# Optimization experiments

Measured on AMD Instinct MI355X. Metric: run time of the kernel, lower is better.

## Reference

```python
import jax, jax.numpy as jnp
import numpy as np
from jax import lax

B, N, C, P = 4, 20000, 21, 100           # batch, anchors, classes (incl. background), proposal_count
SCORE_THR = 0.7
SIGMA = 0.5                              # soft_nms=True -> soft_nms_sigma = 0.5
CLIP_RATIO = 16.0 / 1000.0
BIG = 1e9                                # sentinel for invalid / removed boxes
MAX_RATIO = float(abs(np.log(CLIP_RATIO)))


def setup_inputs() -> dict:
    key = jax.random.key(0)
    k1, k2, k3, k4, k5 = jax.random.split(key, 5)
    score = jax.random.uniform(k1, (B, N, 1), dtype=jnp.float32)
    logits = jax.random.uniform(k2, (B, N, C), dtype=jnp.float32)
    regress = jax.random.normal(k3, (B, N, 4), dtype=jnp.float32) * 0.2
    ctr = jax.random.uniform(k4, (N, 2), minval=0.05, maxval=0.95)
    size = jax.random.uniform(k5, (N, 2), minval=0.02, maxval=0.3)
    anchors = jnp.clip(jnp.concatenate([ctr - 0.5 * size, ctr + 0.5 * size], axis=-1), 0.0, 1.0)
    return {"score": score, "logits": logits, "regress": regress, "anchors": anchors.astype(jnp.float32)}


def _decode(anchors, regress):
    # delta2bbox-style decode (yolo2bbox) with wh-ratio clipping, boxes clipped to [0,1]
    ax1, ay1, ax2, ay2 = anchors[:, 0], anchors[:, 1], anchors[:, 2], anchors[:, 3]
    aw, ah = ax2 - ax1, ay2 - ay1
    acx, acy = ax1 + 0.5 * aw, ay1 + 0.5 * ah
    dx, dy = regress[:, 0], regress[:, 1]
    dw = jnp.clip(regress[:, 2], -MAX_RATIO, MAX_RATIO)
    dh = jnp.clip(regress[:, 3], -MAX_RATIO, MAX_RATIO)
    cx, cy = acx + dx * aw, acy + dy * ah
    w, h = aw * jnp.exp(dw), ah * jnp.exp(dh)
    boxes = jnp.stack([cx - 0.5 * w, cy - 0.5 * h, cx + 0.5 * w, cy + 0.5 * h], axis=-1)
    return jnp.clip(boxes, 0.0, 1.0)


def _iou_one(b, boxes):
    # IoU of one box [4] vs all boxes [N,4]
    x1 = jnp.maximum(b[0], boxes[:, 0])
    y1 = jnp.maximum(b[1], boxes[:, 1])
    x2 = jnp.minimum(b[2], boxes[:, 2])
    y2 = jnp.minimum(b[3], boxes[:, 3])
    inter = jnp.clip(x2 - x1, 0.0) * jnp.clip(y2 - y1, 0.0)
    a = (b[2] - b[0]) * (b[3] - b[1])
    areas = (boxes[:, 2] - boxes[:, 0]) * (boxes[:, 3] - boxes[:, 1])
    return inter / (a + areas - inter + 1e-9)


def _soft_nms(boxes, scores0):
    # Gaussian soft-NMS (TF non_max_suppression_with_scores, soft_nms_sigma>0):
    # weight = exp(-0.5*iou^2/sigma); iou_threshold is ignored in soft mode.
    n = scores0.shape[0]
    ar = jnp.arange(n)

    @jax.checkpoint
    def step(carry, _):
        s, removed = carry
        m = jnp.where(removed, -BIG, s)
        i = jnp.argmax(m)
        valid = m[i] > 0.0
        w = jnp.exp(-0.5 * jnp.square(_iou_one(boxes[i], boxes)) / SIGMA)
        s = jnp.where(valid, s * w, s)
        removed = removed | (ar == i)
        return (s, removed), (i, valid)

    _, (idx, val) = lax.scan(step, (scores0, jnp.zeros(n, bool)), None, length=P)
    return idx, val


def _image(score, logits, regress, anchors):
    le = score * logits                       # [N,C] combined class scores
    label = jnp.argmax(le, axis=-1)
    ms = jnp.max(le, axis=-1)
    valid = (ms >= SCORE_THR) & (label > 0)   # drop background / low score
    boxes = _decode(anchors, regress)         # [N,4]
    cls_scores = jnp.where(valid[None, :], le.T[1:], -BIG)   # [C-1,N]
    idx, val = jax.vmap(_soft_nms, in_axes=(None, 0))(boxes, cls_scores)  # [C-1,P]
    cls = jnp.broadcast_to(jnp.arange(1, C)[:, None], (C - 1, P))
    idx, val, cls = idx.reshape(-1), val.reshape(-1), cls.reshape(-1)
    cand = jnp.where(val, le[idx, cls], -BIG)  # gather_nd on un-decayed logit
    top_s, top_i = lax.top_k(cand, P)          # global top-k over all classes
    fi = idx[top_i]
    ok = (top_s > -BIG / 2)[:, None]
    logit_out = jnp.where(ok, le[fi], 0.0)     # zero-padded like tf.pad
    proposal = jnp.where(ok, boxes[fi], 0.0)
    return logit_out, proposal                 # [P,C], [P,4]


def reference(score, logits, regress, anchors):
    return jax.vmap(_image, in_axes=(0, 0, 0, None))(score, logits, regress, anchors)
```

## Files before the change

kernel.cpp:

```cpp
#include <hip/hip_runtime.h>
#include <climits>
#include <cstdint>

namespace {
constexpr int B = 4, N = 20000, C = 21, P = 100, NC = 20;
constexpr float THR  = 0.7f;
constexpr float BIGF = 1.0e9f;
constexpr float MAXR = 4.135166556742356f;
constexpr float TAU  = 0.8f;
constexpr int NMT  = 512;
constexpr int PCAP = NMT;
constexpr int TKN  = 2048;
constexpr int TKT  = 512;
constexpr int NB   = (N + 255) / 256;
constexpr int GPB  = 2;
constexpr int GB   = (NB + GPB - 1) / GPB;

constexpr size_t OFF_CPACK = 0;
constexpr size_t OFF_MASK  = OFF_CPACK + (size_t)B * N * 32;
constexpr size_t OFF_BCNT  = OFF_MASK  + (size_t)B * N * 4;
constexpr size_t OFF_VCNT  = OFF_BCNT  + 2048;
constexpr size_t OFF_OIDX  = OFF_VCNT  + 64;
constexpr size_t OFF_OVAL  = OFF_OIDX  + (size_t)B * NC * P * 4;
constexpr size_t OFF_OSC   = OFF_OVAL  + (size_t)B * NC * P * 4;
constexpr size_t OFF_OBOX  = OFF_OSC   + (size_t)B * NC * P * 4;
constexpr size_t OFF_SFALL = OFF_OBOX  + (size_t)B * NC * P * 16;
}

template <int CTRL, int RM>
__device__ __forceinline__ float dpp_fmax(float x) {
  int t = __builtin_amdgcn_update_dpp(__float_as_int(x), __float_as_int(x),
                                      CTRL, RM, 0xF, false);
  return fmaxf(x, __int_as_float(t));
}
__device__ __forceinline__ float wave_fmax64(float x) {
  x = dpp_fmax<0x111, 0xF>(x);
  x = dpp_fmax<0x112, 0xF>(x);
  x = dpp_fmax<0x114, 0xF>(x);
  x = dpp_fmax<0x118, 0xF>(x);
  x = dpp_fmax<0x142, 0xA>(x);
  x = dpp_fmax<0x143, 0xC>(x);
  return __int_as_float(__builtin_amdgcn_readlane(__float_as_int(x), 63));
}
__device__ __forceinline__ float fast_rcp(float x) {
  return __builtin_amdgcn_rcpf(x);
}
__device__ __forceinline__ float fast_exp2(float x) {
  return __builtin_amdgcn_exp2f(x);
}
__device__ __forceinline__ unsigned fmap(float v) {
  unsigned u = __float_as_uint(v);
  return (u & 0x80000000u) ? ~u : (u | 0x80000000u);
}
__device__ __forceinline__ float funmap(unsigned u) {
  return __uint_as_float((u & 0x80000000u) ? (u ^ 0x80000000u) : ~u);
}

__global__ __launch_bounds__(256) void k_valid(
    const float* __restrict__ score, const float* __restrict__ logits,
    unsigned* __restrict__ mask, int* __restrict__ bcnt) {
  __shared__ int ws[4];
  int tid = threadIdx.x;
  int n = blockIdx.x * 256 + tid;
  int b = blockIdx.y;
  unsigned mk = 0;
  if (n < N) {
    int bn = b * N + n;
    float sc = score[bn];
    const float* lg = logits + (size_t)bn * C;
    float le[C];
    float ms = -INFINITY;
    int lab = 0;
    #pragma unroll
    for (int c = 0; c < C; ++c) {
      le[c] = __fmul_rn(sc, lg[c]);
      if (le[c] > ms) { ms = le[c]; lab = c; }
    }
    if (ms >= THR && lab > 0) {
      mk = 1u << 20;
      #pragma unroll
      for (int c = 1; c < C; ++c)
        if (le[c] >= TAU) mk |= 1u << (c - 1);
    }
    mask[bn] = mk;
  }
  unsigned long long vb = __ballot(mk != 0);
  if ((tid & 63) == 0) ws[tid >> 6] = __popcll(vb);
  __syncthreads();
  if (tid == 0) bcnt[b * NB + blockIdx.x] = ws[0] + ws[1] + ws[2] + ws[3];
}

__global__ __launch_bounds__(256) void k_compact(
    const float* __restrict__ score, const float* __restrict__ regress,
    const float* __restrict__ anchors, const unsigned* __restrict__ mask,
    const int* __restrict__ bcnt, float* __restrict__ cpack,
    int* __restrict__ vcnt) {
  __shared__ int s_base[4], s_tot[4], s_scan[4];
  int g = blockIdx.x, b = blockIdx.y;
  int tid = threadIdx.x, lane = tid & 63, wid = tid >> 6;
  int idx0 = g * GPB;
  int bv = (tid < idx0) ? bcnt[b * NB + tid] : 0;
  int tv = (tid < NB) ? bcnt[b * NB + tid] : 0;
  #pragma unroll
  for (int off = 32; off; off >>= 1) {
    bv += __shfl_down(bv, off);
    tv += __shfl_down(tv, off);
  }
  if (lane == 0) { s_base[wid] = bv; s_tot[wid] = tv; }
  __syncthreads();
  int base = s_base[0] + s_base[1] + s_base[2] + s_base[3];
  if (g == 0 && tid == 0) vcnt[b] = s_tot[0] + s_tot[1] + s_tot[2] + s_tot[3];

  int n0 = g * (GPB * 256) + tid * GPB;
  unsigned bits = 0; int cnt = 0;
  #pragma unroll
  for (int j = 0; j < GPB; ++j) {
    int n = n0 + j;
    if (n < N && (mask[b * N + n] & (1u << 20))) { bits |= 1u << j; cnt++; }
  }
  int inc = cnt;
  #pragma unroll
  for (int off = 1; off < 64; off <<= 1) {
    int o = __shfl_up(inc, off);
    if (lane >= off) inc += o;
  }
  if (lane == 63) s_scan[wid] = inc;
  __syncthreads();
  int woff = 0;
  for (int k = 0; k < wid; ++k) woff += s_scan[k];
  int pos = base + woff + inc - cnt;
  #pragma unroll
  for (int j = 0; j < GPB; ++j) {
    if (!((bits >> j) & 1u)) continue;
    int n = n0 + j;
    int bn = b * N + n;
    const float* an = anchors + (size_t)n * 4;
    float ax1 = an[0], ay1 = an[1], ax2 = an[2], ay2 = an[3];
    float aw = __fsub_rn(ax2, ax1), ah = __fsub_rn(ay2, ay1);
    float acx = __fadd_rn(ax1, __fmul_rn(0.5f, aw));
    float acy = __fadd_rn(ay1, __fmul_rn(0.5f, ah));
    const float* rg = regress + (size_t)bn * 4;
    float dx = rg[0], dy = rg[1];
    float dw = fminf(fmaxf(rg[2], -MAXR), MAXR);
    float dh = fminf(fmaxf(rg[3], -MAXR), MAXR);
    float cx = __fadd_rn(acx, __fmul_rn(dx, aw));
    float cy = __fadd_rn(acy, __fmul_rn(dy, ah));
    float w = __fmul_rn(aw, expf(dw));
    float h = __fmul_rn(ah, expf(dh));
    float hw = __fmul_rn(0.5f, w), hh = __fmul_rn(0.5f, h);
    float x1 = fminf(fmaxf(__fsub_rn(cx, hw), 0.f), 1.f);
    float y1 = fminf(fmaxf(__fsub_rn(cy, hh), 0.f), 1.f);
    float x2 = fminf(fmaxf(__fadd_rn(cx, hw), 0.f), 1.f);
    float y2 = fminf(fmaxf(__fadd_rn(cy, hh), 0.f), 1.f);
    float area = __fmul_rn(__fsub_rn(x2, x1), __fsub_rn(y2, y1));
    unsigned mk = mask[bn];
    float4* cp = reinterpret_cast<float4*>(cpack) + ((size_t)b * N + pos) * 2;
    cp[0] = make_float4(x1, y1, x2, y2);
    cp[1] = make_float4(__int_as_float(n), score[bn], area, __uint_as_float(mk));
    pos++;
  }
}

__global__ __launch_bounds__(NMT) void k_nms(
    const float* __restrict__ logits, const float* __restrict__ cpack,
    const int* __restrict__ vcnt, float* __restrict__ sfall,
    int* __restrict__ oidx, int* __restrict__ oval,
    float* __restrict__ osc, float* __restrict__ obox) {
  constexpr int NW = NMT / 64;
  __shared__ float4 s_box[PCAP];
  __shared__ float  s_ar[PCAP], s_s[PCAP];
  __shared__ int    s_n[PCAP];
  __shared__ int    s_selj[P];
  __shared__ int    s_wcnt[NW];
  __shared__ int    s_fail;
  __shared__ unsigned long long s_key[2][NW];
  __shared__ float  s_red[NW];
  __shared__ int    s_redi[NW];

  int blk = blockIdx.x;
  int b = blk / NC;
  int cls = blk % NC + 1;
  int V = vcnt[b];
  int tid = threadIdx.x;
  int lane = tid & 63, wid = tid >> 6;
  const float* cpf = cpack + (size_t)b * N * 8;
  int* oi = oidx + (size_t)blk * P;
  int* ov = oval + (size_t)blk * P;
  float* os = osc + (size_t)blk * P;
  float4* ob = reinterpret_cast<float4*>(obox) + (size_t)blk * P;
  unsigned clsbit = 1u << (cls - 1);

  s_box[tid] = make_float4(0.f, 0.f, 0.f, 0.f);

  int ch = (V + NMT - 1) / NMT;
  int v0 = tid * ch, v1 = min(v0 + ch, V);
  int cnt = 0;
  for (int v = v0; v < v1; ++v) {
    unsigned mk = __float_as_uint(cpf[(size_t)v * 8 + 7]);
    if (mk & clsbit) cnt++;
  }
  int inc = cnt;
  #pragma unroll
  for (int off = 1; off < 64; off <<= 1) {
    int o = __shfl_up(inc, off);
    if (lane >= off) inc += o;
  }
  if (lane == 63) s_wcnt[wid] = inc;
  __syncthreads();
  int woff = 0;
  for (int k = 0; k < wid; ++k) woff += s_wcnt[k];
  int pcnt = 0;
  #pragma unroll
  for (int k = 0; k < NW; ++k) pcnt += s_wcnt[k];
  int pos = woff + inc - cnt;
  for (int v = v0; v < v1; ++v) {
    const float4* cp = reinterpret_cast<const float4*>(cpf) + (size_t)v * 2;
    float4 f2 = cp[1];
    unsigned mk = __float_as_uint(f2.w);
    if (mk & clsbit) {
      if (pos < PCAP) {
        float4 f1 = cp[0];
        int n = __float_as_int(f2.x);
        float lg = logits[(size_t)(b * N + n) * C + cls];
        s_s[pos]   = __fmul_rn(f2.y, lg);
        s_box[pos] = f1;
        s_ar[pos]  = f2.z;
        s_n[pos]   = n;
      }
      pos++;
    }
  }
  __syncthreads();

  bool fail0 = (pcnt > PCAP);
  if (!fail0) {
    bool in = tid < pcnt;
    float4 q = s_box[tid];
    float sr = in ? s_s[tid] : -INFINITY;
    float qx = q.x, qy = q.y, qz = q.z, qw = q.w;
    float pa = in ? s_ar[tid] : 0.f;
    float gmax = -INFINITY;

    for (int t = 0; t < P; ++t) {
      int par = t & 1;
      float lm = wave_fmax64(sr);
      unsigned long long bm = __ballot(sr == lm);
      int lane_w = __ffsll(bm) - 1;
      if (lane == 0)
        s_key[par][wid] = ((unsigned long long)fmap(lm) << 32) |
                          (unsigned)(~(unsigned)(wid * 64 + lane_w));
      __syncthreads();
      unsigned long long kb = s_key[par][0];
      #pragma unroll
      for (int k = 1; k < NW; ++k) {
        unsigned long long kk = s_key[par][k];
        kb = (kk > kb) ? kk : kb;
      }
      gmax = funmap((unsigned)(kb >> 32));
      int j_w = (int)(~(unsigned)kb);
      if (tid == 0) s_selj[t] = j_w;
      float4 wbx = s_box[j_w];
      float wa = __fmul_rn(__fsub_rn(wbx.z, wbx.x),
                           __fsub_rn(wbx.w, wbx.y));
      float s1 = __fadd_rn(wa, 1e-9f);
      float x1 = fmaxf(wbx.x, qx), y1 = fmaxf(wbx.y, qy);
      float x2 = fminf(wbx.z, qz), y2 = fminf(wbx.w, qw);
      float iw = fmaxf(__fsub_rn(x2, x1), 0.f);
      float ih = fmaxf(__fsub_rn(y2, y1), 0.f);
      float inter = __fmul_rn(iw, ih);
      float den = __fsub_rn(__fadd_rn(pa, s1), inter);
      float iou = __fmul_rn(inter, fast_rcp(den));
      float m2 = __fmul_rn(__fmul_rn(iou, iou), -1.44269504089f);
      float wgt = fast_exp2(m2);
      float ns = __fmul_rn(sr, wgt);
      sr = (tid == j_w) ? -INFINITY : ns;
    }
    if (tid == 0) s_fail = (gmax < TAU) ? 1 : 0;
    __syncthreads();
    if (!s_fail) {
      if (tid < P) {
        int wj = s_selj[tid];
        oi[tid] = s_n[wj];
        ov[tid] = 1;
        os[tid] = s_s[wj];
        ob[tid] = s_box[wj];
      }
      return;
    }
  }

  __syncthreads();
  float* sg = sfall + (size_t)blk * N;
  for (int v = tid; v < V; v += NMT) {
    const float* c2 = cpf + (size_t)v * 8 + 4;
    int n = __float_as_int(c2[0]);
    sg[v] = __fmul_rn(c2[1], logits[(size_t)(b * N + n) * C + cls]);
  }
  __syncthreads();

  for (int t = 0; t < P; ++t) {
    float bv = -INFINITY; int bi = INT_MAX;
    for (int v = tid; v < V; v += NMT) {
      float sv = sg[v];
      if (sv > bv) { bv = sv; bi = v; }
    }
    #pragma unroll
    for (int off = 32; off; off >>= 1) {
      float ovv = __shfl_down(bv, off); int oii = __shfl_down(bi, off);
      if (ovv > bv || (ovv == bv && oii < bi)) { bv = ovv; bi = oii; }
    }
    if (lane == 0) { s_red[wid] = bv; s_redi[wid] = bi; }
    __syncthreads();
    float wv = -INFINITY; int wi = INT_MAX;
    #pragma unroll
    for (int k = 0; k < NW; ++k) {
      float v = s_red[k]; int i = s_redi[k];
      if (v > wv || (v == wv && i < wi)) { wv = v; wi = i; }
    }
    __syncthreads();
    if (wi == INT_MAX) {
      if (tid == 0) for (int u = t; u < P; ++u) {
        oi[u] = 0; ov[u] = 0; os[u] = 0.f;
        ob[u] = make_float4(0.f, 0.f, 0.f, 0.f);
      }
      break;
    }
    int vd = (wv > 0.0f) ? 1 : 0;
    const float* cw = cpf + (size_t)wi * 8;
    if (tid == 0) {
      int n = __float_as_int(cw[4]);
      oi[t] = n; ov[t] = vd;
      os[t] = __fmul_rn(cw[5], logits[(size_t)(b * N + n) * C + cls]);
      ob[t] = make_float4(cw[0], cw[1], cw[2], cw[3]);
    }
    float w0, w1, w2, w3;
    if (vd) { w0 = cw[0]; w1 = cw[1]; w2 = cw[2]; w3 = cw[3]; }
    else    { w0 = w1 = w2 = w3 = 0.f; }
    float wa = __fmul_rn(__fsub_rn(w2, w0), __fsub_rn(w3, w1));
    for (int v = tid; v < V; v += NMT) {
      float sv = (v == wi) ? -INFINITY : sg[v];
      const float* cq = cpf + (size_t)v * 8;
      float x1 = fmaxf(w0, cq[0]), y1 = fmaxf(w1, cq[1]);
      float x2 = fminf(w2, cq[2]), y2 = fminf(w3, cq[3]);
      float iw = fmaxf(__fsub_rn(x2, x1), 0.f);
      float ih = fmaxf(__fsub_rn(y2, y1), 0.f);
      float inter = __fmul_rn(iw, ih);
      float den = __fadd_rn(__fsub_rn(__fadd_rn(wa, cq[6]), inter), 1e-9f);
      float iou = __fdiv_rn(inter, den);
      float wgt = expf(-__fmul_rn(iou, iou));
      sg[v] = __fmul_rn(sv, wgt);
    }
    __syncthreads();
  }
}

__global__ __launch_bounds__(TKT) void k_topk(
    const float* __restrict__ score, const float* __restrict__ logits,
    const float* __restrict__ obox, const int* __restrict__ oidx,
    const int* __restrict__ oval, const float* __restrict__ osc,
    float* __restrict__ out) {
  __shared__ unsigned long long s_key[TKN];
  __shared__ int s_fi[TKN];

  int b = blockIdx.x;
  int tid = threadIdx.x;
  size_t base = (size_t)b * NC * P;

  #pragma unroll
  for (int q = 0; q < TKN / TKT; ++q) {
    int j = tid + q * TKT;
    unsigned hi;
    if (j < NC * P) {
      int vl = oval[base + j];
      float c = vl ? osc[base + j] : -BIGF;
      s_fi[j] = oidx[base + j];
      hi = fmap(c);
    } else {
      s_fi[j] = 0;
      hi = fmap(-INFINITY);
    }
    s_key[j] = ((unsigned long long)hi << 32) | (unsigned)(~j);
  }

  for (int k = 2; k <= TKN; k <<= 1) {
    for (int j = k >> 1; j > 0; j >>= 1) {
      __syncthreads();
      #pragma unroll
      for (int q = 0; q < TKN / 2 / TKT; ++q) {
        int p = tid + q * TKT;
        int i = ((p & ~(j - 1)) << 1) | (p & (j - 1));
        int l = i | j;
        unsigned long long a = s_key[i], bb = s_key[l];
        bool desc = ((i & k) == 0);
        if (desc ? (a < bb) : (a > bb)) { s_key[i] = bb; s_key[l] = a; }
      }
    }
  }
  __syncthreads();

  for (int kk = tid; kk < P * C; kk += TKT) {
    int t = kk / C, cls = kk % C;
    unsigned long long kt = s_key[t];
    float sv = funmap((unsigned)(kt >> 32));
    int j = (int)(~(unsigned)kt);
    bool okp = sv > -BIGF * 0.5f;
    float o = 0.f;
    if (okp) {
      int fi = s_fi[j];
      int bn = b * N + fi;
      o = __fmul_rn(score[bn], logits[(size_t)bn * C + cls]);
    }
    out[((size_t)b * P + t) * C + cls] = o;
  }
  for (int kk = tid; kk < P * 4; kk += TKT) {
    int t = kk / 4, d = kk % 4;
    unsigned long long kt = s_key[t];
    float sv = funmap((unsigned)(kt >> 32));
    int j = (int)(~(unsigned)kt);
    bool okp = sv > -BIGF * 0.5f;
    float o = 0.f;
    if (okp) o = obox[(base + j) * 4 + d];
    out[(size_t)B * P * C + ((size_t)b * P + t) * 4 + d] = o;
  }
}

extern "C" void kernel_launch(void* const* d_in, const int* in_sizes, int n_in,
                              void* d_out, int out_size, void* d_ws, size_t ws_size,
                              hipStream_t stream) {
  const float* score   = (const float*)d_in[0];
  const float* logits  = (const float*)d_in[1];
  const float* regress = (const float*)d_in[2];
  const float* anchors = (const float*)d_in[3];
  float* out = (float*)d_out;

  char* ws = (char*)d_ws;
  float*    cpack = (float*)(ws + OFF_CPACK);
  unsigned* mask  = (unsigned*)(ws + OFF_MASK);
  int*      bcnt  = (int*)(ws + OFF_BCNT);
  int*      vcnt  = (int*)(ws + OFF_VCNT);
  int*      oidx  = (int*)(ws + OFF_OIDX);
  int*      oval  = (int*)(ws + OFF_OVAL);
  float*    osc   = (float*)(ws + OFF_OSC);
  float*    obox  = (float*)(ws + OFF_OBOX);
  float*    sfall = (float*)(ws + OFF_SFALL);

  k_valid<<<dim3(NB, B), 256, 0, stream>>>(score, logits, mask, bcnt);
  k_compact<<<dim3(GB, B), 256, 0, stream>>>(score, regress, anchors, mask,
                                             bcnt, cpack, vcnt);
  k_nms<<<B * NC, NMT, 0, stream>>>(logits, cpack, vcnt, sfall, oidx, oval,
                                    osc, obox);
  k_topk<<<B, TKT, 0, stream>>>(score, logits, obox, oidx, oval, osc, out);
}
```

Baseline: 92.27 us.

## Halve NMS block size, two candidates per thread, broadcast winner box via readlane

The soft-NMS block drops from 512 to 256 threads. Each thread now holds two candidate boxes and scores, so the candidate capacity stays at 512. Each wave picks its local winner, reads that winner's box, area and index with readlane, and publishes them to shared memory. After the barrier, every thread reduces the four wave entries and gets the winning box directly, instead of doing a separate shared-memory lookup of s_box[j_w]. This aims to shorten the serial per-iteration critical path: fewer waves at each barrier, a smaller cross-wave reduction and no dependent LDS load. The cost is doubled per-thread IoU work and more register pressure.

```diff
diff --git a/kernel.cpp b/kernel.cpp
--- a/kernel.cpp
+++ b/kernel.cpp
@@ -8,8 +8,8 @@
 constexpr float BIGF = 1.0e9f;
 constexpr float MAXR = 4.135166556742356f;
 constexpr float TAU  = 0.8f;
-constexpr int NMT  = 512;
-constexpr int PCAP = NMT;
+constexpr int NMT  = 256;
+constexpr int PCAP = 512;
 constexpr int TKN  = 2048;
 constexpr int TKT  = 512;
 constexpr int NB   = (N + 255) / 256;
@@ -41,6 +41,12 @@
   x = dpp_fmax<0x142, 0xA>(x);
   x = dpp_fmax<0x143, 0xC>(x);
   return __int_as_float(__builtin_amdgcn_readlane(__float_as_int(x), 63));
+}
+__device__ __forceinline__ float rlane_f(float x, int l) {
+  return __int_as_float(__builtin_amdgcn_readlane(__float_as_int(x), l));
+}
+__device__ __forceinline__ int rlane_i(int x, int l) {
+  return __builtin_amdgcn_readlane(x, l);
 }
 __device__ __forceinline__ float fast_rcp(float x) {
   return __builtin_amdgcn_rcpf(x);
@@ -173,7 +179,8 @@
   __shared__ int    s_selj[P];
   __shared__ int    s_wcnt[NW];
   __shared__ int    s_fail;
-  __shared__ unsigned long long s_key[2][NW];
+  __shared__ float4 s_puba[2][NW];
+  __shared__ float4 s_pubb[2][NW];
   __shared__ float  s_red[NW];
   __shared__ int    s_redi[NW];
 
@@ -191,6 +198,7 @@
   unsigned clsbit = 1u << (cls - 1);
 
   s_box[tid] = make_float4(0.f, 0.f, 0.f, 0.f);
+  s_box[tid + 256] = make_float4(0.f, 0.f, 0.f, 0.f);
 
   int ch = (V + NMT - 1) / NMT;
   int v0 = tid * ch, v1 = min(v0 + ch, V);
@@ -234,46 +242,90 @@
 
   bool fail0 = (pcnt > PCAP);
   if (!fail0) {
-    bool in = tid < pcnt;
-    float4 q = s_box[tid];
-    float sr = in ? s_s[tid] : -INFINITY;
-    float qx = q.x, qy = q.y, qz = q.z, qw = q.w;
-    float pa = in ? s_ar[tid] : 0.f;
+    int j0 = 128 * wid + 2 * lane;
+    int j1 = j0 + 1;
+    float4 q0 = s_box[j0], q1 = s_box[j1];
+    float sr0 = (j0 < pcnt) ? s_s[j0] : -INFINITY;
+    float sr1 = (j1 < pcnt) ? s_s[j1] : -INFINITY;
+    float pa0 = (j0 < pcnt) ? s_ar[j0] : 0.f;
+    float pa1 = (j1 < pcnt) ? s_ar[j1] : 0.f;
     float gmax = -INFINITY;
 
     for (int t = 0; t < P; ++t) {
       int par = t & 1;
-      float lm = wave_fmax64(sr);
-      unsigned long long bm = __ballot(sr == lm);
+      bool sel1 = sr1 > sr0;
+      float lm = sel1 ? sr1 : sr0;
+      float wm = wave_fmax64(lm);
+      unsigned long long bm = __ballot(lm == wm);
       int lane_w = __ffsll(bm) - 1;
-      if (lane == 0)
-        s_key[par][wid] = ((unsigned long long)fmap(lm) << 32) |
-                          (unsigned)(~(unsigned)(wid * 64 + lane_w));
+      int   mj  = sel1 ? j1 : j0;
+      float cx1 = sel1 ? q1.x : q0.x;
+      float cy1 = sel1 ? q1.y : q0.y;
+      float cx2 = sel1 ? q1.z : q0.z;
+      float cy2 = sel1 ? q1.w : q0.w;
+      float ca  = sel1 ? pa1 : pa0;
+      int   jw  = rlane_i(mj, lane_w);
+      float bx1 = rlane_f(cx1, lane_w), by1 = rlane_f(cy1, lane_w);
+      float bx2 = rlane_f(cx2, lane_w), by2 = rlane_f(cy2, lane_w);
+      float ba  = rlane_f(ca, lane_w);
+      if (lane == 0) {
+        s_puba[par][wid] = make_float4(
+            __uint_as_float(~(unsigned)jw), __uint_as_float(fmap(wm)),
+            __fadd_rn(ba, 1e-9f), 0.f);
+        s_pubb[par][wid] = make_float4(bx1, by1, bx2, by2);
+      }
       __syncthreads();
-      unsigned long long kb = s_key[par][0];
-      #pragma unroll
-      for (int k = 1; k < NW; ++k) {
-        unsigned long long kk = s_key[par][k];
-        kb = (kk > kb) ? kk : kb;
-      }
+      float4 a0 = s_puba[par][0], a1 = s_puba[par][1];
+      float4 a2 = s_puba[par][2], a3 = s_puba[par][3];
+      float4 p0 = s_pubb[par][0], p1 = s_pubb[par][1];
+      float4 p2 = s_pubb[par][2], p3 = s_pubb[par][3];
+      unsigned long long k0 =
+          ((unsigned long long)__float_as_uint(a0.y) << 32) | __float_as_uint(a0.x);
+      unsigned long long k1 =
+          ((unsigned long long)__float_as_uint(a1.y) << 32) | __float_as_uint(a1.x);
+      unsigned long long k2 =
+          ((unsigned long long)__float_as_uint(a2.y) << 32) | __float_as_uint(a2.x);
+      unsigned long long k3 =
+          ((unsigned long long)__float_as_uint(a3.y) << 32) | __float_as_uint(a3.x);
+      unsigned long long kb = k0; float4 wb = p0; float s1 = a0.z;
+      { bool g = k1 > kb; kb = g ? k1 : kb; s1 = g ? a1.z : s1;
+        wb.x = g ? p1.x : wb.x; wb.y = g ? p1.y : wb.y;
+        wb.z = g ? p1.z : wb.z; wb.w = g ? p1.w : wb.w; }
+      { bool g = k2 > kb; kb = g ? k2 : kb; s1 = g ? a2.z : s1;
+        wb.x = g ? p2.x : wb.x; wb.y = g ? p2.y : wb.y;
+        wb.z = g ? p2.z : wb.z; wb.w = g ? p2.w : wb.w; }
+      { bool g = k3 > kb; kb = g ? k3 : kb; s1 = g ? a3.z : s1;
+        wb.x = g ? p3.x : wb.x; wb.y = g ? p3.y : wb.y;
+        wb.z = g ? p3.z : wb.z; wb.w = g ? p3.w : wb.w; }
       gmax = funmap((unsigned)(kb >> 32));
       int j_w = (int)(~(unsigned)kb);
       if (tid == 0) s_selj[t] = j_w;
-      float4 wbx = s_box[j_w];
-      float wa = __fmul_rn(__fsub_rn(wbx.z, wbx.x),
-                           __fsub_rn(wbx.w, wbx.y));
-      float s1 = __fadd_rn(wa, 1e-9f);
-      float x1 = fmaxf(wbx.x, qx), y1 = fmaxf(wbx.y, qy);
-      float x2 = fminf(wbx.z, qz), y2 = fminf(wbx.w, qw);
-      float iw = fmaxf(__fsub_rn(x2, x1), 0.f);
-      float ih = fmaxf(__fsub_rn(y2, y1), 0.f);
-      float inter = __fmul_rn(iw, ih);
-      float den = __fsub_rn(__fadd_rn(pa, s1), inter);
-      float iou = __fmul_rn(inter, fast_rcp(den));
-      float m2 = __fmul_rn(__fmul_rn(iou, iou), -1.44269504089f);
-      float wgt = fast_exp2(m2);
-      float ns = __fmul_rn(sr, wgt);
-      sr = (tid == j_w) ? -INFINITY : ns;
+      {
+        float x1 = fmaxf(wb.x, q0.x), y1 = fmaxf(wb.y, q0.y);
+        float x2 = fminf(wb.z, q0.z), y2 = fminf(wb.w, q0.w);
+        float iw = fmaxf(__fsub_rn(x2, x1), 0.f);
+        float ih = fmaxf(__fsub_rn(y2, y1), 0.f);
+        float inter = __fmul_rn(iw, ih);
+        float den = __fsub_rn(__fadd_rn(pa0, s1), inter);
+        float iou = __fmul_rn(inter, fast_rcp(den));
+        float m2 = __fmul_rn(__fmul_rn(iou, iou), -1.44269504089f);
+        float wgt = fast_exp2(m2);
+        float ns = __fmul_rn(sr0, wgt);
+        sr0 = (j0 == j_w) ? -INFINITY : ns;
+      }
+      {
+        float x1 = fmaxf(wb.x, q1.x), y1 = fmaxf(wb.y, q1.y);
+        float x2 = fminf(wb.z, q1.z), y2 = fminf(wb.w, q1.w);
+        float iw = fmaxf(__fsub_rn(x2, x1), 0.f);
+        float ih = fmaxf(__fsub_rn(y2, y1), 0.f);
+        float inter = __fmul_rn(iw, ih);
+        float den = __fsub_rn(__fadd_rn(pa1, s1), inter);
+        float iou = __fmul_rn(inter, fast_rcp(den));
+        float m2 = __fmul_rn(__fmul_rn(iou, iou), -1.44269504089f);
+        float wgt = fast_exp2(m2);
+        float ns = __fmul_rn(sr1, wgt);
+        sr1 = (j1 == j_w) ? -INFINITY : ns;
+      }
     }
     if (tid == 0) s_fail = (gmax < TAU) ? 1 : 0;
     __syncthreads();
```

Result: slower. 104.0 us (+12.8%).

## Select two soft-NMS winners per round when top boxes don't overlap

Applied to the files above, without the earlier changes.

Each soft-NMS round now finds the top two candidates per wave and merges top-2 keys across waves. When the best and second-best boxes have zero intersection, the second's score is unaffected by the first decay, so both are selected in one round. This halves barrier and reduction rounds in the favorable case. It adds a second wave reduction and a larger merge per round, which is extra cost when overlaps force single selection.

```diff
diff --git a/kernel.cpp b/kernel.cpp
--- a/kernel.cpp
+++ b/kernel.cpp
@@ -173,7 +173,7 @@
   __shared__ int    s_selj[P];
   __shared__ int    s_wcnt[NW];
   __shared__ int    s_fail;
-  __shared__ unsigned long long s_key[2][NW];
+  __shared__ unsigned long long s_pk[2][NW][2];
   __shared__ float  s_red[NW];
   __shared__ int    s_redi[NW];
 
@@ -239,43 +239,89 @@
     float sr = in ? s_s[tid] : -INFINITY;
     float qx = q.x, qy = q.y, qz = q.z, qw = q.w;
     float pa = in ? s_ar[tid] : 0.f;
-    float gmax = -INFINITY;
-
-    for (int t = 0; t < P; ++t) {
-      int par = t & 1;
-      float lm = wave_fmax64(sr);
-      unsigned long long bm = __ballot(sr == lm);
-      int lane_w = __ffsll(bm) - 1;
-      if (lane == 0)
-        s_key[par][wid] = ((unsigned long long)fmap(lm) << 32) |
-                          (unsigned)(~(unsigned)(wid * 64 + lane_w));
+    float lastG = -INFINITY;
+
+#define NMS_DECAY(bb, s1v) {                                                 \
+      float x1 = fmaxf(bb.x, qx), y1 = fmaxf(bb.y, qy);                      \
+      float x2 = fminf(bb.z, qz), y2 = fminf(bb.w, qw);                      \
+      float iw = fmaxf(__fsub_rn(x2, x1), 0.f);                              \
+      float ih = fmaxf(__fsub_rn(y2, y1), 0.f);                              \
+      float inter = __fmul_rn(iw, ih);                                       \
+      float den = __fsub_rn(__fadd_rn(pa, s1v), inter);                      \
+      float iou = __fmul_rn(inter, fast_rcp(den));                           \
+      float m2 = __fmul_rn(__fmul_rn(iou, iou), -1.44269504089f);            \
+      float wgt = fast_exp2(m2);                                             \
+      sr = __fmul_rn(sr, wgt); }
+
+#define NMS_MRG(o1, o2, a1, a2, b1, b2) {                                    \
+      bool c = (a1) > (b1);                                                  \
+      unsigned long long lo = c ? (b1) : (a1);                               \
+      unsigned long long al = c ? (a2) : (b2);                               \
+      o1 = c ? (a1) : (b1);                                                  \
+      o2 = (lo > al) ? lo : al; }
+
+    int t = 0, r = 0;
+    while (t < P) {
+      int par = r & 1; r++;
+      float wm1 = wave_fmax64(sr);
+      unsigned long long bm1 = __ballot(sr == wm1);
+      int lw1 = __ffsll(bm1) - 1;
+      float l2 = (lane == lw1) ? -INFINITY : sr;
+      float wm2 = wave_fmax64(l2);
+      unsigned long long bm2 = __ballot(l2 == wm2);
+      int lw2 = __ffsll(bm2) - 1;
+      if (lane == lw1)
+        s_pk[par][wid][0] = ((unsigned long long)fmap(wm1) << 32) |
+                            (unsigned)(~(unsigned)tid);
+      if (lane == lw2)
+        s_pk[par][wid][1] = ((unsigned long long)fmap(wm2) << 32) |
+                            (unsigned)(~(unsigned)tid);
       __syncthreads();
-      unsigned long long kb = s_key[par][0];
-      #pragma unroll
-      for (int k = 1; k < NW; ++k) {
-        unsigned long long kk = s_key[par][k];
-        kb = (kk > kb) ? kk : kb;
+      ulonglong2 p0 = *reinterpret_cast<ulonglong2*>(&s_pk[par][0][0]);
+      ulonglong2 p1 = *reinterpret_cast<ulonglong2*>(&s_pk[par][1][0]);
+      ulonglong2 p2 = *reinterpret_cast<ulonglong2*>(&s_pk[par][2][0]);
+      ulonglong2 p3 = *reinterpret_cast<ulonglong2*>(&s_pk[par][3][0]);
+      ulonglong2 p4 = *reinterpret_cast<ulonglong2*>(&s_pk[par][4][0]);
+      ulonglong2 p5 = *reinterpret_cast<ulonglong2*>(&s_pk[par][5][0]);
+      ulonglong2 p6 = *reinterpret_cast<ulonglong2*>(&s_pk[par][6][0]);
+      ulonglong2 p7 = *reinterpret_cast<ulonglong2*>(&s_pk[par][7][0]);
+      unsigned long long a1, a2, c1, c2, e1, e2, g1k, g2k;
+      NMS_MRG(a1, a2, p0.x, p0.y, p1.x, p1.y)
+      NMS_MRG(c1, c2, p2.x, p2.y, p3.x, p3.y)
+      NMS_MRG(e1, e2, p4.x, p4.y, p5.x, p5.y)
+      NMS_MRG(g1k, g2k, p6.x, p6.y, p7.x, p7.y)
+      unsigned long long h1, h2, i1, i2, K1, K2;
+      NMS_MRG(h1, h2, a1, a2, c1, c2)
+      NMS_MRG(i1, i2, e1, e2, g1k, g2k)
+      NMS_MRG(K1, K2, h1, h2, i1, i2)
+      int j1 = (int)(~(unsigned)K1);
+      int j2 = (int)(~(unsigned)K2);
+      float4 b1 = s_box[j1];
+      float4 b2 = s_box[j2];
+      float wa1 = __fmul_rn(__fsub_rn(b1.z, b1.x), __fsub_rn(b1.w, b1.y));
+      float s11 = __fadd_rn(wa1, 1e-9f);
+      float ox1 = fmaxf(b1.x, b2.x), oy1 = fmaxf(b1.y, b2.y);
+      float ox2 = fminf(b1.z, b2.z), oy2 = fminf(b1.w, b2.w);
+      float oiw = fmaxf(__fsub_rn(ox2, ox1), 0.f);
+      float oih = fmaxf(__fsub_rn(oy2, oy1), 0.f);
+      bool ok2 = (__fmul_rn(oiw, oih) == 0.0f) && (t + 1 < P);
+      NMS_DECAY(b1, s11)
+      if (tid == j1) sr = -INFINITY;
+      if (tid == 0) s_selj[t] = j1;
+      lastG = funmap((unsigned)(K1 >> 32));
+      if (ok2) {
+        float wa2 = __fmul_rn(__fsub_rn(b2.z, b2.x), __fsub_rn(b2.w, b2.y));
+        float s12 = __fadd_rn(wa2, 1e-9f);
+        NMS_DECAY(b2, s12)
+        if (tid == j2) sr = -INFINITY;
+        if (tid == 0) s_selj[t + 1] = j2;
+        lastG = funmap((unsigned)(K2 >> 32));
+        t += 2;
+      } else {
+        t += 1;
       }
-      gmax = funmap((unsigned)(kb >> 32));
-      int j_w = (int)(~(unsigned)kb);
-      if (tid == 0) s_selj[t] = j_w;
-      float4 wbx = s_box[j_w];
-      float wa = __fmul_rn(__fsub_rn(wbx.z, wbx.x),
-                           __fsub_rn(wbx.w, wbx.y));
-      float s1 = __fadd_rn(wa, 1e-9f);
-      float x1 = fmaxf(wbx.x, qx), y1 = fmaxf(wbx.y, qy);
-      float x2 = fminf(wbx.z, qz), y2 = fminf(wbx.w, qw);
-      float iw = fmaxf(__fsub_rn(x2, x1), 0.f);
-      float ih = fmaxf(__fsub_rn(y2, y1), 0.f);
-      float inter = __fmul_rn(iw, ih);
-      float den = __fsub_rn(__fadd_rn(pa, s1), inter);
-      float iou = __fmul_rn(inter, fast_rcp(den));
-      float m2 = __fmul_rn(__fmul_rn(iou, iou), -1.44269504089f);
-      float wgt = fast_exp2(m2);
-      float ns = __fmul_rn(sr, wgt);
-      sr = (tid == j_w) ? -INFINITY : ns;
-    }
-    if (tid == 0) s_fail = (gmax < TAU) ? 1 : 0;
+    }
+    if (tid == 0) s_fail = (lastG < TAU) ? 1 : 0;
     __syncthreads();
     if (!s_fail) {
       if (tid < P) {
```

Measured after the change: 113.0 us. +22.5%, slower.

## Use LDS atomicMax for NMS argmax and register/shuffle bitonic sort in top-k

Applied to the files above, without the earlier changes.

In the soft-NMS loop, each wave now folds its per-wave max into a single shared 64-bit key with atomicMax. The key is tagged with the iteration number so it never needs resetting, which replaces the per-wave key array and the serial 8-way scan. The top-k kernel's bitonic sort of 2048 keys now keeps 4 keys per thread in registers, uses wave shuffles for small strides and LDS exchanges only for strides crossing waves. This cuts most of the __syncthreads barriers and shared-memory traffic. The risks are packing the score into 32 bits of a 41-bit field and the more intricate sort-stage indexing.

```diff
diff --git a/kernel.cpp b/kernel.cpp
--- a/kernel.cpp
+++ b/kernel.cpp
@@ -173,7 +173,7 @@
   __shared__ int    s_selj[P];
   __shared__ int    s_wcnt[NW];
   __shared__ int    s_fail;
-  __shared__ unsigned long long s_key[2][NW];
+  __shared__ unsigned long long s_gk[2];
   __shared__ float  s_red[NW];
   __shared__ int    s_redi[NW];
 
@@ -191,6 +191,7 @@
   unsigned clsbit = 1u << (cls - 1);
 
   s_box[tid] = make_float4(0.f, 0.f, 0.f, 0.f);
+  if (tid == 0) { s_gk[0] = 0ull; s_gk[1] = 0ull; }
 
   int ch = (V + NMT - 1) / NMT;
   int v0 = tid * ch, v1 = min(v0 + ch, V);
@@ -239,25 +240,23 @@
     float sr = in ? s_s[tid] : -INFINITY;
     float qx = q.x, qy = q.y, qz = q.z, qw = q.w;
     float pa = in ? s_ar[tid] : 0.f;
-    float gmax = -INFINITY;
+    unsigned long long kb = 0ull;
 
     for (int t = 0; t < P; ++t) {
       int par = t & 1;
       float lm = wave_fmax64(sr);
       unsigned long long bm = __ballot(sr == lm);
       int lane_w = __ffsll(bm) - 1;
-      if (lane == 0)
-        s_key[par][wid] = ((unsigned long long)fmap(lm) << 32) |
-                          (unsigned)(~(unsigned)(wid * 64 + lane_w));
+      if (lane == 0) {
+        unsigned inv = 511u - (unsigned)(wid * 64 + lane_w);
+        unsigned long long key = ((unsigned long long)(t + 1) << 41) |
+                                 ((unsigned long long)fmap(lm) << 9) |
+                                 (unsigned long long)inv;
+        atomicMax(&s_gk[par], key);
+      }
       __syncthreads();
-      unsigned long long kb = s_key[par][0];
-      #pragma unroll
-      for (int k = 1; k < NW; ++k) {
-        unsigned long long kk = s_key[par][k];
-        kb = (kk > kb) ? kk : kb;
-      }
-      gmax = funmap((unsigned)(kb >> 32));
-      int j_w = (int)(~(unsigned)kb);
+      kb = s_gk[par];
+      int j_w = 511 - (int)((unsigned)kb & 511u);
       if (tid == 0) s_selj[t] = j_w;
       float4 wbx = s_box[j_w];
       float wa = __fmul_rn(__fsub_rn(wbx.z, wbx.x),
@@ -275,6 +274,7 @@
       float ns = __fmul_rn(sr, wgt);
       sr = (tid == j_w) ? -INFINITY : ns;
     }
+    float gmax = funmap((unsigned)((kb >> 9) & 0xFFFFFFFFull));
     if (tid == 0) s_fail = (gmax < TAU) ? 1 : 0;
     __syncthreads();
     if (!s_fail) {
@@ -359,44 +359,111 @@
     const float* __restrict__ obox, const int* __restrict__ oidx,
     const int* __restrict__ oval, const float* __restrict__ osc,
     float* __restrict__ out) {
-  __shared__ unsigned long long s_key[TKN];
+  __shared__ unsigned long long s_k2[2][TKN];
   __shared__ int s_fi[TKN];
 
   int b = blockIdx.x;
   int tid = threadIdx.x;
   size_t base = (size_t)b * NC * P;
 
-  #pragma unroll
-  for (int q = 0; q < TKN / TKT; ++q) {
-    int j = tid + q * TKT;
-    unsigned hi;
-    if (j < NC * P) {
-      int vl = oval[base + j];
-      float c = vl ? osc[base + j] : -BIGF;
-      s_fi[j] = oidx[base + j];
-      hi = fmap(c);
+  unsigned long long v0, v1, v2, v3;
+  {
+    int j0 = 4 * tid;
+    if (j0 + 3 < NC * P) {
+      int4   vl4 = *reinterpret_cast<const int4*>(oval + base + j0);
+      float4 sc4 = *reinterpret_cast<const float4*>(osc + base + j0);
+      int4   fi4 = *reinterpret_cast<const int4*>(oidx + base + j0);
+      s_fi[j0]     = fi4.x; s_fi[j0 + 1] = fi4.y;
+      s_fi[j0 + 2] = fi4.z; s_fi[j0 + 3] = fi4.w;
+      v0 = ((unsigned long long)fmap(vl4.x ? sc4.x : -BIGF) << 32) |
+           (unsigned)(~(j0 + 0));
+      v1 = ((unsigned long long)fmap(vl4.y ? sc4.y : -BIGF) << 32) |
+           (unsigned)(~(j0 + 1));
+      v2 = ((unsigned long long)fmap(vl4.z ? sc4.z : -BIGF) << 32) |
+           (unsigned)(~(j0 + 2));
+      v3 = ((unsigned long long)fmap(vl4.w ? sc4.w : -BIGF) << 32) |
+           (unsigned)(~(j0 + 3));
     } else {
-      s_fi[j] = 0;
-      hi = fmap(-INFINITY);
-    }
-    s_key[j] = ((unsigned long long)hi << 32) | (unsigned)(~j);
-  }
-
-  for (int k = 2; k <= TKN; k <<= 1) {
-    for (int j = k >> 1; j > 0; j >>= 1) {
-      __syncthreads();
-      #pragma unroll
-      for (int q = 0; q < TKN / 2 / TKT; ++q) {
-        int p = tid + q * TKT;
-        int i = ((p & ~(j - 1)) << 1) | (p & (j - 1));
-        int l = i | j;
-        unsigned long long a = s_key[i], bb = s_key[l];
-        bool desc = ((i & k) == 0);
-        if (desc ? (a < bb) : (a > bb)) { s_key[i] = bb; s_key[l] = a; }
-      }
-    }
-  }
-  __syncthreads();
+      s_fi[j0] = 0; s_fi[j0 + 1] = 0; s_fi[j0 + 2] = 0; s_fi[j0 + 3] = 0;
+      unsigned long long hi = (unsigned long long)fmap(-INFINITY) << 32;
+      v0 = hi | (unsigned)(~(j0 + 0));
+      v1 = hi | (unsigned)(~(j0 + 1));
+      v2 = hi | (unsigned)(~(j0 + 2));
+      v3 = hi | (unsigned)(~(j0 + 3));
+    }
+  }
+
+  auto cmpx = [](unsigned long long& a, unsigned long long pv, bool keepmax) {
+    bool agt = a > pv;
+    a = (keepmax == agt) ? a : pv;
+  };
+  auto shfl_stage = [&](int k, int j) {
+    int xd = j >> 2;
+    bool up = ((tid & xd) == 0);
+    bool desc = ((tid & (k >> 2)) == 0);
+    bool keepmax = (up == desc);
+    unsigned long long p0 = __shfl_xor(v0, xd);
+    unsigned long long p1 = __shfl_xor(v1, xd);
+    unsigned long long p2 = __shfl_xor(v2, xd);
+    unsigned long long p3 = __shfl_xor(v3, xd);
+    cmpx(v0, p0, keepmax); cmpx(v1, p1, keepmax);
+    cmpx(v2, p2, keepmax); cmpx(v3, p3, keepmax);
+  };
+  auto reg_stage = [&](int k) {
+    bool desc = ((tid & (k >> 2)) == 0);
+    auto sw = [&](unsigned long long& a, unsigned long long& bb) {
+      if (desc ? (a < bb) : (a > bb)) { unsigned long long t = a; a = bb; bb = t; }
+    };
+    sw(v0, v2); sw(v1, v3);
+    sw(v0, v1); sw(v2, v3);
+  };
+  auto lds_stage = [&](int k, int j, int par) {
+    unsigned long long* buf = s_k2[par];
+    int j0 = 4 * tid;
+    buf[j0] = v0; buf[j0 + 1] = v1; buf[j0 + 2] = v2; buf[j0 + 3] = v3;
+    __syncthreads();
+    int pj = 4 * (tid ^ (j >> 2));
+    unsigned long long p0 = buf[pj], p1 = buf[pj + 1];
+    unsigned long long p2 = buf[pj + 2], p3 = buf[pj + 3];
+    bool up = ((tid & (j >> 2)) == 0);
+    bool desc = ((tid & (k >> 2)) == 0);
+    bool keepmax = (up == desc);
+    cmpx(v0, p0, keepmax); cmpx(v1, p1, keepmax);
+    cmpx(v2, p2, keepmax); cmpx(v3, p3, keepmax);
+  };
+
+  { if (v0 < v1) { unsigned long long t = v0; v0 = v1; v1 = t; }
+    if (v2 > v3) { unsigned long long t = v2; v2 = v3; v3 = t; } }
+  reg_stage(4);
+  #pragma unroll
+  for (int k = 8; k <= 256; k <<= 1) {
+    #pragma unroll
+    for (int j = k >> 1; j >= 4; j >>= 1) shfl_stage(k, j);
+    reg_stage(k);
+  }
+  lds_stage(512, 256, 0);
+  #pragma unroll
+  for (int j = 128; j >= 4; j >>= 1) shfl_stage(512, j);
+  reg_stage(512);
+  lds_stage(1024, 512, 1);
+  lds_stage(1024, 256, 0);
+  #pragma unroll
+  for (int j = 128; j >= 4; j >>= 1) shfl_stage(1024, j);
+  reg_stage(1024);
+  lds_stage(2048, 1024, 1);
+  lds_stage(2048, 512, 0);
+  lds_stage(2048, 256, 1);
+  #pragma unroll
+  for (int j = 128; j >= 4; j >>= 1) shfl_stage(2048, j);
+  reg_stage(2048);
+
+  {
+    int j0 = 4 * tid;
+    unsigned long long* buf = s_k2[0];
+    buf[j0] = v0; buf[j0 + 1] = v1; buf[j0 + 2] = v2; buf[j0 + 3] = v3;
+  }
+  __syncthreads();
+  const unsigned long long* s_key = s_k2[0];
 
   for (int kk = tid; kk < P * C; kk += TKT) {
     int t = kk / C, cls = kk % C;
```

After: 79.17 us. 14.2% less time.
